# Optimization experiments

Hardware: AMD Instinct MI355X
Metric: run time of the kernel (lower is better)

## Reference

```python
import jax, jax.numpy as jnp
import numpy as np

DIM = 1024
HEADS = 16
DIM_HEAD = 64


def setup_inputs() -> dict:
    key = jax.random.key(0)
    ks = jax.random.split(key, 6)
    b, n = 2, 2048
    x = jax.random.normal(ks[0], (b, n, DIM), dtype=jnp.float32)
    gamma = jnp.ones((DIM,), dtype=jnp.float32)
    w_qkv = jax.random.normal(ks[1], (DIM, 3 * HEADS * DIM_HEAD), dtype=jnp.float32) * (DIM ** -0.5)
    w_gates = jax.random.normal(ks[2], (DIM, HEADS), dtype=jnp.float32) * (DIM ** -0.5)
    b_gates = jnp.zeros((HEADS,), dtype=jnp.float32)
    w_out = jax.random.normal(ks[3], (HEADS * DIM_HEAD, DIM), dtype=jnp.float32) * ((HEADS * DIM_HEAD) ** -0.5)
    freqs = jax.random.uniform(ks[4], (DIM_HEAD // 2,), dtype=jnp.float32)
    return {"x": x, "gamma": gamma, "w_qkv": w_qkv, "w_gates": w_gates,
            "b_gates": b_gates, "w_out": w_out, "freqs": freqs}


def _rotate_half(t):
    # interleaved pairs: (x1, x2) -> (-x2, x1)
    tp = t.reshape(t.shape[:-1] + (t.shape[-1] // 2, 2))
    x1, x2 = tp[..., 0], tp[..., 1]
    return jnp.stack((-x2, x1), axis=-1).reshape(t.shape)


def reference(x, gamma, w_qkv, w_gates, b_gates, w_out, freqs):
    b, n, d = x.shape
    # RMSNorm variant: divide by L2 norm, scale by gamma * sqrt(dim)
    xn = x / jnp.linalg.norm(x, axis=-1, keepdims=True)
    xn = xn * gamma * (d ** 0.5)
    # QKV projection: (b, n, 3*H*D) -> q,k,v each (b, h, n, dh)
    qkv = xn @ w_qkv
    qkv = qkv.reshape(b, n, 3, HEADS, DIM_HEAD).transpose(2, 0, 3, 1, 4)
    q, k, v = qkv[0], qkv[1], qkv[2]
    # Inline RoPE (interleaved): freqs (n, dh)
    pos = jnp.arange(n, dtype=freqs.dtype)
    f = jnp.repeat(pos[:, None] * freqs[None, :], 2, axis=-1)  # (n, dh)
    cos_f, sin_f = jnp.cos(f), jnp.sin(f)
    q = q * cos_f + _rotate_half(q) * sin_f
    k = k * cos_f + _rotate_half(k) * sin_f
    # SDPA
    scale = DIM_HEAD ** -0.5
    scores = jnp.einsum('bhqd,bhkd->bhqk', q, k) * scale
    attn = jax.nn.softmax(scores, axis=-1)
    out = jnp.einsum('bhqk,bhkd->bhqd', attn, v)  # (b, h, n, dh)
    # per-head sigmoid gate from normalized input
    gates = xn @ w_gates + b_gates  # (b, n, h)
    out = out * jax.nn.sigmoid(gates.transpose(0, 2, 1))[..., None]
    # merge heads and output projection
    out = out.transpose(0, 2, 1, 3).reshape(b, n, HEADS * DIM_HEAD)
    return out @ w_out
```

## Files before the change

### kernel.cpp

```cpp
#include <hip/hip_runtime.h>

typedef __bf16 bf16_t;
typedef __bf16 bf16x8 __attribute__((ext_vector_type(8)));
typedef __bf16 bf16x4 __attribute__((ext_vector_type(4)));
typedef float f32x4 __attribute__((ext_vector_type(4)));

#define B_  2
#define N_  2048
#define D_  1024
#define H_  16
#define DH_ 64

#define QSCALE 0.18033688011112042f
#define NEGC  -11.541560327111707f

#if __has_builtin(__builtin_amdgcn_exp2f)
#define EXP2F(x) __builtin_amdgcn_exp2f(x)
#else
#define EXP2F(x) exp2f(x)
#endif

#define GLL16(g, l) __builtin_amdgcn_global_load_lds( \
    (const __attribute__((address_space(1))) void*)(g), \
    (__attribute__((address_space(3))) void*)(l), 16, 0, 0)

__device__ __forceinline__ int xcd_swizzle_id() {
  int id = blockIdx.y * gridDim.x + blockIdx.x;
  int cpx = (gridDim.x * gridDim.y) >> 3;
  return (id & 7) * cpx + (id >> 3);
}

__global__ __launch_bounds__(256) void k_trig(const float* __restrict__ freqs,
    float* __restrict__ tc, float* __restrict__ ts) {
  int idx = blockIdx.x * 256 + threadIdx.x;
  int n = idx >> 5, j = idx & 31;
  float f = (float)n * freqs[j];
  tc[idx] = cosf(f);
  ts[idx] = sinf(f);
}

__global__ __launch_bounds__(256) void k_rmsnorm_gates(const float* __restrict__ x,
    const float* __restrict__ gamma, const float* __restrict__ wg,
    const float* __restrict__ bg, bf16_t* __restrict__ xn, float* __restrict__ gsig) {
  int row = blockIdx.x;
  const float4* xr = (const float4*)(x + (size_t)row * D_);
  int tid = threadIdx.x;
  float4 v = xr[tid];
  float ss = v.x*v.x + v.y*v.y + v.z*v.z + v.w*v.w;
  #pragma unroll
  for (int off = 32; off > 0; off >>= 1) ss += __shfl_down(ss, off);
  __shared__ float red4[4];
  if ((tid & 63) == 0) red4[tid >> 6] = ss;
  __syncthreads();
  float scale = 32.0f * rsqrtf(red4[0] + red4[1] + red4[2] + red4[3]);
  float4 g = ((const float4*)gamma)[tid];
  bf16x4 o;
  o[0] = (bf16_t)(v.x * scale * g.x);
  o[1] = (bf16_t)(v.y * scale * g.y);
  o[2] = (bf16_t)(v.z * scale * g.z);
  o[3] = (bf16_t)(v.w * scale * g.w);
  *(bf16x4*)(xn + (size_t)row * D_ + tid * 4) = o;
  float xv[4] = {(float)o[0], (float)o[1], (float)o[2], (float)o[3]};
  float part[16];
  #pragma unroll
  for (int h = 0; h < 16; ++h) part[h] = 0.f;
  #pragma unroll
  for (int j = 0; j < 4; ++j) {
    const float4* wr = (const float4*)&wg[(size_t)(tid * 4 + j) * 16];
    #pragma unroll
    for (int q = 0; q < 4; ++q) {
      float4 w4 = wr[q];
      part[q * 4 + 0] += xv[j] * w4.x;
      part[q * 4 + 1] += xv[j] * w4.y;
      part[q * 4 + 2] += xv[j] * w4.z;
      part[q * 4 + 3] += xv[j] * w4.w;
    }
  }
  __shared__ float red[256][17];
  #pragma unroll
  for (int h = 0; h < 16; ++h) red[tid][h] = part[h];
  __syncthreads();
  int h = tid & 15, grp = tid >> 4;
  float s = 0.f;
  #pragma unroll
  for (int k = 0; k < 16; ++k) s += red[grp * 16 + k][h];
  __syncthreads();
  red[grp][h] = s;
  __syncthreads();
  if (tid < 16) {
    float acc = bg[tid];
    #pragma unroll
    for (int k = 0; k < 16; ++k) acc += red[k][tid];
    gsig[(size_t)row * 16 + tid] = 1.0f / (1.0f + __expf(-acc));
  }
}

__global__ __launch_bounds__(256) void k_transpose_cvt(const float* __restrict__ W,
    bf16_t* __restrict__ Wt, int R, int C) {
  __shared__ float tile[32][33];
  int c0 = blockIdx.x * 32, r0 = blockIdx.y * 32;
  int tx = threadIdx.x & 31, ty = threadIdx.x >> 5;
  #pragma unroll
  for (int i = 0; i < 4; ++i) {
    int r = ty + i * 8;
    tile[r][tx] = W[(size_t)(r0 + r) * C + c0 + tx];
  }
  __syncthreads();
  #pragma unroll
  for (int i = 0; i < 4; ++i) {
    int rr = ty + i * 8;
    Wt[(size_t)(c0 + rr) * R + r0 + tx] = (bf16_t)tile[tx][rr];
  }
}

__global__ __launch_bounds__(256) void k_gemm_qkv(const bf16_t* __restrict__ A,
    const bf16_t* __restrict__ Bt, const float* __restrict__ tc,
    const float* __restrict__ ts, bf16_t* __restrict__ Qb,
    bf16_t* __restrict__ Kb, bf16_t* __restrict__ Vb) {
  constexpr int BK = 32, K = 1024;
  __shared__ __align__(16) bf16_t As[128 * BK];
  __shared__ __align__(16) bf16_t Bs[128 * BK];
  int tid = threadIdx.x, wave = tid >> 6, lane = tid & 63;
  int l16 = lane & 15, quad = lane >> 4;
  int swz = xcd_swizzle_id();
  int bxi = swz % 32, byi = swz / 32;
  int bm = bxi * 128, bn = byi * 128;
  int wm = (wave >> 1) * 64, wn = (wave & 1) * 64;
  int srow = wave * 32 + (lane >> 2);
  int scol = (lane & 3) * 8;
  const bf16_t* gA0 = &A [(size_t)(bm + srow)      * K + scol];
  const bf16_t* gA1 = &A [(size_t)(bm + srow + 16) * K + scol];
  const bf16_t* gB0 = &Bt[(size_t)(bn + srow)      * K + scol];
  const bf16_t* gB1 = &Bt[(size_t)(bn + srow + 16) * K + scol];
  bf16_t* lA0 = &As[(wave * 32)      * BK];
  bf16_t* lA1 = &As[(wave * 32 + 16) * BK];
  bf16_t* lB0 = &Bs[(wave * 32)      * BK];
  bf16_t* lB1 = &Bs[(wave * 32 + 16) * BK];
  f32x4 acc[4][4] = {};
  for (int k0 = 0; k0 < K; k0 += BK) {
    GLL16(gA0 + k0, lA0);
    GLL16(gA1 + k0, lA1);
    GLL16(gB0 + k0, lB0);
    GLL16(gB1 + k0, lB1);
    __syncthreads();
    bf16x8 af[4], bfr[4];
    #pragma unroll
    for (int t = 0; t < 4; ++t) {
      af[t]  = *(const bf16x8*)&As[(wm + t * 16 + l16) * BK + quad * 8];
      bfr[t] = *(const bf16x8*)&Bs[(wn + t * 16 + l16) * BK + quad * 8];
    }
    #pragma unroll
    for (int mt = 0; mt < 4; ++mt)
      #pragma unroll
      for (int nt = 0; nt < 4; ++nt)
        acc[mt][nt] = __builtin_amdgcn_mfma_f32_16x16x32_bf16(af[mt], bfr[nt], acc[mt][nt], 0, 0, 0);
    __syncthreads();
  }
  if (byi < 16) {
    float qs = (byi < 8) ? QSCALE : 1.0f;
    bf16_t* dst = (byi < 8) ? Qb : Kb;
    #pragma unroll
    for (int mt = 0; mt < 4; ++mt)
      #pragma unroll
      for (int r = 0; r < 4; ++r) {
        int row = bm + wm + mt * 16 + quad * 4 + r;
        int b = row >> 11, n = row & 2047;
        const float* cr = tc + n * 32;
        const float* sr = ts + n * 32;
        #pragma unroll
        for (int nt = 0; nt < 4; ++nt) {
          int col = bn + wn + nt * 16 + l16;
          int h = (col >> 6) & 15, d = col & 63, j = d >> 1;
          float val = acc[mt][nt][r];
          float p = __shfl_xor(val, 1);
          float c = cr[j], s = sr[j];
          float o = (d & 1) ? (val * c + p * s) : (val * c - p * s);
          dst[((size_t)(b * H_ + h) * N_ + n) * DH_ + d] = (bf16_t)(o * qs);
        }
      }
  } else {
    #pragma unroll
    for (int mt = 0; mt < 4; ++mt)
      #pragma unroll
      for (int nt = 0; nt < 4; ++nt) {
        int row0 = bm + wm + mt * 16 + quad * 4;
        int b = row0 >> 11, n0 = row0 & 2047;
        int col = bn + wn + nt * 16 + l16;
        int h = (col >> 6) & 15, d = col & 63;
        bf16x4 pk;
        #pragma unroll
        for (int r = 0; r < 4; ++r) pk[r] = (bf16_t)acc[mt][nt][r];
        *(bf16x4*)&Vb[((size_t)(b * H_ + h) * DH_ + d) * N_ + n0] = pk;
      }
  }
}

__global__ __launch_bounds__(256) void k_gemm_bt_n64(const bf16_t* __restrict__ A,
    const bf16_t* __restrict__ Bt, float* __restrict__ C, int M, int N, int K) {
  constexpr int BK = 32;
  __shared__ __align__(16) bf16_t As[128 * BK];
  __shared__ __align__(16) bf16_t Bs[64 * BK];
  int tid = threadIdx.x, wave = tid >> 6, lane = tid & 63;
  int l16 = lane & 15, quad = lane >> 4;
  int swz = xcd_swizzle_id();
  int bxi = swz % gridDim.x, byi = swz / gridDim.x;
  int bm = bxi * 128, bn = byi * 64;
  int wm = (wave >> 1) * 64, wn = (wave & 1) * 32;
  int srow = wave * 32 + (lane >> 2);
  int scol = (lane & 3) * 8;
  const bf16_t* gA0 = &A [(size_t)(bm + srow)      * K + scol];
  const bf16_t* gA1 = &A [(size_t)(bm + srow + 16) * K + scol];
  int srB = wave * 16 + (lane >> 2);
  const bf16_t* gB0 = &Bt[(size_t)(bn + srB) * K + scol];
  bf16_t* lA0 = &As[(wave * 32)      * BK];
  bf16_t* lA1 = &As[(wave * 32 + 16) * BK];
  bf16_t* lB0 = &Bs[(wave * 16)      * BK];
  f32x4 acc[4][2] = {};
  for (int k0 = 0; k0 < K; k0 += BK) {
    GLL16(gA0 + k0, lA0);
    GLL16(gA1 + k0, lA1);
    GLL16(gB0 + k0, lB0);
    __syncthreads();
    bf16x8 af[4], bfr[2];
    #pragma unroll
    for (int t = 0; t < 4; ++t)
      af[t]  = *(const bf16x8*)&As[(wm + t * 16 + l16) * BK + quad * 8];
    #pragma unroll
    for (int t = 0; t < 2; ++t)
      bfr[t] = *(const bf16x8*)&Bs[(wn + t * 16 + l16) * BK + quad * 8];
    #pragma unroll
    for (int mt = 0; mt < 4; ++mt)
      #pragma unroll
      for (int nt = 0; nt < 2; ++nt)
        acc[mt][nt] = __builtin_amdgcn_mfma_f32_16x16x32_bf16(af[mt], bfr[nt], acc[mt][nt], 0, 0, 0);
    __syncthreads();
  }
  #pragma unroll
  for (int mt = 0; mt < 4; ++mt)
    #pragma unroll
    for (int nt = 0; nt < 2; ++nt)
      #pragma unroll
      for (int r = 0; r < 4; ++r) {
        int row = bm + wm + mt * 16 + quad * 4 + r;
        int col = bn + wn + nt * 16 + l16;
        C[(size_t)row * N + col] = acc[mt][nt][r];
      }
}

__global__ __launch_bounds__(256) void k_flash(const bf16_t* __restrict__ Qb,
    const bf16_t* __restrict__ Kb, const bf16_t* __restrict__ Vb,
    const float* __restrict__ gsig, bf16_t* __restrict__ Ao) {
  __shared__ __align__(16) bf16_t Ks[2][64 * 72];
  __shared__ __align__(16) bf16_t Vt[2][64 * 72];
  __shared__ __align__(16) bf16_t Ps[4][32 * 72];
  int swz = xcd_swizzle_id();
  int qblk = swz & 15, bh = swz >> 4;
  int b = bh >> 4, h = bh & 15;
  int tid = threadIdx.x, wave = tid >> 6, lane = tid & 63;
  int l16 = lane & 15, quad = lane >> 4;
  int qw = qblk * 128 + wave * 32;
  const bf16_t* Qh = Qb + (size_t)bh * N_ * DH_;
  const bf16_t* Kh = Kb + (size_t)bh * N_ * DH_;
  const bf16_t* Vh = Vb + (size_t)bh * DH_ * N_;
  bf16_t* Pw = Ps[wave];
  bf16x8 qf[2][2];
  #pragma unroll
  for (int qt = 0; qt < 2; ++qt)
    #pragma unroll
    for (int hf = 0; hf < 2; ++hf)
      qf[qt][hf] = *(const bf16x8*)&Qh[(size_t)(qw + qt * 16 + l16) * DH_ + hf * 32 + quad * 8];
  bf16x8 onesf;
  #pragma unroll
  for (int i = 0; i < 8; ++i) onesf[i] = (bf16_t)1.0f;
  f32x4 accO[2][4] = {};
  f32x4 accL[2] = {};
  int sk = tid >> 3;
  int sc = (tid & 7) * 8;
  bf16x8 rk0 = *(const bf16x8*)&Kh[(size_t)sk * DH_ + sc];
  bf16x8 rk1 = *(const bf16x8*)&Kh[(size_t)(sk + 32) * DH_ + sc];
  bf16x8 rv0 = *(const bf16x8*)&Vh[(size_t)sk * N_ + sc];
  bf16x8 rv1 = *(const bf16x8*)&Vh[(size_t)(sk + 32) * N_ + sc];
  *(bf16x8*)&Ks[0][sk * 72 + sc]        = rk0;
  *(bf16x8*)&Ks[0][(sk + 32) * 72 + sc] = rk1;
  *(bf16x8*)&Vt[0][sk * 72 + sc]        = rv0;
  *(bf16x8*)&Vt[0][(sk + 32) * 72 + sc] = rv1;
  __syncthreads();
  const f32x4 zinit = {NEGC, NEGC, NEGC, NEGC};
  for (int k0 = 0; k0 < N_; k0 += 64) {
    int cur = (k0 >> 6) & 1;
    const bf16_t* Kc = Ks[cur];
    const bf16_t* Vc = Vt[cur];
    int kn = k0 + 64;
    if (kn < N_) {
      rk0 = *(const bf16x8*)&Kh[(size_t)(kn + sk) * DH_ + sc];
      rk1 = *(const bf16x8*)&Kh[(size_t)(kn + sk + 32) * DH_ + sc];
      rv0 = *(const bf16x8*)&Vh[(size_t)sk * N_ + kn + sc];
      rv1 = *(const bf16x8*)&Vh[(size_t)(sk + 32) * N_ + kn + sc];
    }
    f32x4 st[4][2];
    __builtin_amdgcn_s_setprio(1);
    #pragma unroll
    for (int kt = 0; kt < 4; ++kt) {
      bf16x8 kf0 = *(const bf16x8*)&Kc[(kt * 16 + l16) * 72 + quad * 8];
      bf16x8 kf1 = *(const bf16x8*)&Kc[(kt * 16 + l16) * 72 + 32 + quad * 8];
      #pragma unroll
      for (int qt = 0; qt < 2; ++qt) {
        f32x4 z = zinit;
        z = __builtin_amdgcn_mfma_f32_16x16x32_bf16(kf0, qf[qt][0], z, 0, 0, 0);
        z = __builtin_amdgcn_mfma_f32_16x16x32_bf16(kf1, qf[qt][1], z, 0, 0, 0);
        st[kt][qt] = z;
      }
    }
    __builtin_amdgcn_s_setprio(0);
    #pragma unroll
    for (int qt = 0; qt < 2; ++qt)
      #pragma unroll
      for (int kt = 0; kt < 4; ++kt) {
        bf16x4 pk;
        #pragma unroll
        for (int r = 0; r < 4; ++r)
          pk[r] = (bf16_t)EXP2F(st[kt][qt][r]);
        *(bf16x4*)&Pw[(qt * 16 + l16) * 72 + kt * 16 + quad * 4] = pk;
      }
    bf16x8 pf[2][2];
    #pragma unroll
    for (int qt = 0; qt < 2; ++qt)
      #pragma unroll
      for (int hf = 0; hf < 2; ++hf)
        pf[qt][hf] = *(const bf16x8*)&Pw[(qt * 16 + l16) * 72 + hf * 32 + quad * 8];
    __builtin_amdgcn_s_setprio(1);
    #pragma unroll
    for (int qt = 0; qt < 2; ++qt) {
      accL[qt] = __builtin_amdgcn_mfma_f32_16x16x32_bf16(pf[qt][0], onesf, accL[qt], 0, 0, 0);
      accL[qt] = __builtin_amdgcn_mfma_f32_16x16x32_bf16(pf[qt][1], onesf, accL[qt], 0, 0, 0);
    }
    #pragma unroll
    for (int dt = 0; dt < 4; ++dt)
      #pragma unroll
      for (int hf = 0; hf < 2; ++hf) {
        bf16x8 vf = *(const bf16x8*)&Vc[(dt * 16 + l16) * 72 + hf * 32 + quad * 8];
        #pragma unroll
        for (int qt = 0; qt < 2; ++qt)
          accO[qt][dt] = __builtin_amdgcn_mfma_f32_16x16x32_bf16(pf[qt][hf], vf, accO[qt][dt], 0, 0, 0);
      }
    __builtin_amdgcn_s_setprio(0);
    if (kn < N_) {
      int nb = cur ^ 1;
      *(bf16x8*)&Ks[nb][sk * 72 + sc]        = rk0;
      *(bf16x8*)&Ks[nb][(sk + 32) * 72 + sc] = rk1;
      *(bf16x8*)&Vt[nb][sk * 72 + sc]        = rv0;
      *(bf16x8*)&Vt[nb][(sk + 32) * 72 + sc] = rv1;
    }
    __syncthreads();
  }
  #pragma unroll
  for (int qt = 0; qt < 2; ++qt)
    #pragma unroll
    for (int r = 0; r < 4; ++r) {
      int q = qw + qt * 16 + quad * 4 + r;
      float g = gsig[((size_t)b * N_ + q) * H_ + h];
      float ginv = g / accL[qt][r];
      #pragma unroll
      for (int dt = 0; dt < 4; ++dt)
        Ao[((size_t)b * N_ + q) * (H_ * DH_) + h * DH_ + dt * 16 + l16] =
            (bf16_t)(accO[qt][dt][r] * ginv);
    }
}

extern "C" void kernel_launch(void* const* d_in, const int* in_sizes, int n_in,
                              void* d_out, int out_size, void* d_ws, size_t ws_size,
                              hipStream_t stream) {
  (void)in_sizes; (void)n_in; (void)out_size; (void)ws_size;
  const float* x      = (const float*)d_in[0];
  const float* gamma  = (const float*)d_in[1];
  const float* w_qkv  = (const float*)d_in[2];
  const float* w_gate = (const float*)d_in[3];
  const float* b_gate = (const float*)d_in[4];
  const float* w_out  = (const float*)d_in[5];
  const float* freqs  = (const float*)d_in[6];
  float* out = (float*)d_out;
  char* ws = (char*)d_ws;
  bf16_t* xn    = (bf16_t*)(ws);
  bf16_t* wqkvT = (bf16_t*)(ws + ((size_t)8  << 20));
  bf16_t* woutT = (bf16_t*)(ws + ((size_t)14 << 20));
  bf16_t* Qb    = (bf16_t*)(ws + ((size_t)16 << 20));
  bf16_t* Kb    = (bf16_t*)(ws + ((size_t)24 << 20));
  bf16_t* Vb    = (bf16_t*)(ws + ((size_t)32 << 20));
  float*  gsig  = (float*) (ws + ((size_t)40 << 20));
  bf16_t* attn  = (bf16_t*)(ws + ((size_t)41 << 20));
  float*  trigc = (float*) (ws + ((size_t)49 << 20));
  float*  trigs = (float*) (ws + ((size_t)50 << 20));

  k_trig<<<256, 256, 0, stream>>>(freqs, trigc, trigs);
  k_transpose_cvt<<<dim3(3072 / 32, 1024 / 32), 256, 0, stream>>>(w_qkv, wqkvT, 1024, 3072);
  k_transpose_cvt<<<dim3(1024 / 32, 1024 / 32), 256, 0, stream>>>(w_out, woutT, 1024, 1024);
  k_rmsnorm_gates<<<4096, 256, 0, stream>>>(x, gamma, w_gate, b_gate, xn, gsig);
  k_gemm_qkv<<<dim3(32, 24), 256, 0, stream>>>(xn, wqkvT, trigc, trigs, Qb, Kb, Vb);
  k_flash<<<dim3(16, 32), 256, 0, stream>>>(Qb, Kb, Vb, gsig, attn);
  k_gemm_bt_n64<<<dim3(32, 16), 256, 0, stream>>>(attn, woutT, out, 4096, 1024, 1024);
}
```

Baseline: 242.4 us.

## Stage QKV GEMM epilogue through LDS for coalesced 16-byte stores and remap tiles

The QKV GEMM epilogue now writes RoPE-rotated Q/K and the V tile into a padded shared-memory tile, then issues coalesced 16-byte global stores instead of scattered 2-byte (Q/K) or 8-byte (V transposed) stores. The block-to-tile mapping is also replaced with an explicit XCD-aware layout that groups tiles per XCD for L2 reuse. This adds about 34KB of LDS per block plus an extra barrier, which may reduce occupancy.

```diff
diff --git a/kernel.cpp b/kernel.cpp
--- a/kernel.cpp
+++ b/kernel.cpp
@@ -118,12 +118,16 @@
     const float* __restrict__ ts, bf16_t* __restrict__ Qb,
     bf16_t* __restrict__ Kb, bf16_t* __restrict__ Vb) {
   constexpr int BK = 32, K = 1024;
+  constexpr int TP = 136;
   __shared__ __align__(16) bf16_t As[128 * BK];
   __shared__ __align__(16) bf16_t Bs[128 * BK];
+  __shared__ __align__(16) bf16_t Tt[128 * TP];
   int tid = threadIdx.x, wave = tid >> 6, lane = tid & 63;
   int l16 = lane & 15, quad = lane >> 4;
-  int swz = xcd_swizzle_id();
-  int bxi = swz % 32, byi = swz / 32;
+  int id = blockIdx.y * 32 + blockIdx.x;
+  int xcd = id & 7, local = id >> 3;
+  int bxi = (xcd & 3) * 8 + (local & 7);
+  int byi = (xcd >> 2) * 12 + (local >> 3);
   int bm = bxi * 128, bn = byi * 128;
   int wm = (wave >> 1) * 64, wn = (wave & 1) * 64;
   int srow = wave * 32 + (lane >> 2);
@@ -163,35 +167,52 @@
     for (int mt = 0; mt < 4; ++mt)
       #pragma unroll
       for (int r = 0; r < 4; ++r) {
-        int row = bm + wm + mt * 16 + quad * 4 + r;
-        int b = row >> 11, n = row & 2047;
+        int row_l = wm + mt * 16 + quad * 4 + r;
+        int n = (bm + row_l) & 2047;
         const float* cr = tc + n * 32;
         const float* sr = ts + n * 32;
         #pragma unroll
         for (int nt = 0; nt < 4; ++nt) {
-          int col = bn + wn + nt * 16 + l16;
-          int h = (col >> 6) & 15, d = col & 63, j = d >> 1;
+          int col_l = wn + nt * 16 + l16;
+          int d = (bn + col_l) & 63, j = d >> 1;
           float val = acc[mt][nt][r];
           float p = __shfl_xor(val, 1);
           float c = cr[j], s = sr[j];
           float o = (d & 1) ? (val * c + p * s) : (val * c - p * s);
-          dst[((size_t)(b * H_ + h) * N_ + n) * DH_ + d] = (bf16_t)(o * qs);
+          Tt[row_l * TP + col_l] = (bf16_t)(o * qs);
         }
       }
+    __syncthreads();
+    #pragma unroll
+    for (int it = 0; it < 8; ++it) {
+      int idx = tid + 256 * it;
+      int row_l = idx >> 4, ck = (idx & 15) * 8;
+      bf16x8 v = *(const bf16x8*)&Tt[row_l * TP + ck];
+      int grow = bm + row_l, b = grow >> 11, n = grow & 2047;
+      int col = bn + ck, h = (col >> 6) & 15, d = col & 63;
+      *(bf16x8*)&dst[((size_t)(b * H_ + h) * N_ + n) * DH_ + d] = v;
+    }
   } else {
     #pragma unroll
     for (int mt = 0; mt < 4; ++mt)
       #pragma unroll
       for (int nt = 0; nt < 4; ++nt) {
-        int row0 = bm + wm + mt * 16 + quad * 4;
-        int b = row0 >> 11, n0 = row0 & 2047;
-        int col = bn + wn + nt * 16 + l16;
-        int h = (col >> 6) & 15, d = col & 63;
-        bf16x4 pk;
+        int col_l = wn + nt * 16 + l16;
+        int row0 = wm + mt * 16 + quad * 4;
         #pragma unroll
-        for (int r = 0; r < 4; ++r) pk[r] = (bf16_t)acc[mt][nt][r];
-        *(bf16x4*)&Vb[((size_t)(b * H_ + h) * DH_ + d) * N_ + n0] = pk;
-      }
+        for (int r = 0; r < 4; ++r)
+          Tt[col_l * TP + row0 + r] = (bf16_t)acc[mt][nt][r];
+      }
+    __syncthreads();
+    int b = bm >> 11, nb = bm & 2047;
+    #pragma unroll
+    for (int it = 0; it < 8; ++it) {
+      int idx = tid + 256 * it;
+      int col_l = idx >> 4, ck = (idx & 15) * 8;
+      bf16x8 v = *(const bf16x8*)&Tt[col_l * TP + ck];
+      int vcol = bn + col_l - 2048, h = vcol >> 6, d = vcol & 63;
+      *(bf16x8*)&Vb[((size_t)(b * H_ + h) * DH_ + d) * N_ + nb + ck] = v;
+    }
   }
 }
 
```

Result: no change. 239.7 us (-1.1%).
